# Kernel tuning notes

Hardware: AMD Instinct MI355X
Metric: run time of the kernel (lower is better)

The kernel has to match this reference:

```python
import jax, jax.numpy as jnp
import numpy as np

N, D = 8192, 1024


def setup_inputs() -> dict:
    key = jax.random.key(0)
    k1, k2, k3 = jax.random.split(key, 3)
    f_1 = jax.random.normal(k1, (N, D), dtype=jnp.float32)
    f_2 = jax.random.normal(k2, (N, D), dtype=jnp.float32)
    f_3 = jax.random.normal(k3, (N, D), dtype=jnp.float32)
    return {"f_1": f_1, "f_2": f_2, "f_3": f_3, "batch": 3}


def _svdvals(x):
    # torch.svd computes full U, S, V; only singular values are consumed.
    return jnp.linalg.svd(x, compute_uv=False)


def reference(f_1, f_2, f_3, batch):
    if batch == 2:
        s_1 = _svdvals(f_1)
        if f_2.shape[0] == 0:
            return s_1[0] ** 2
        s_2 = _svdvals(f_2)
        return s_1.mean() + s_2.mean()
    elif batch == 3:
        s_1 = _svdvals(f_1)
        s_2 = _svdvals(f_2)
        s_3 = _svdvals(f_3)
        return s_1[0] ** 2 + 0.5 * (s_2[0] ** 2 + s_3[0] ** 2)
```

## Files before the change

### kernel.cpp

```cpp
#include <hip/hip_runtime.h>


#define DIM 1024
#define NROW 8192
#define MSZ (DIM*DIM)
#define NS 5

typedef __attribute__((ext_vector_type(8))) short short8;
typedef __attribute__((ext_vector_type(4))) float f32x4;

__device__ inline float bf2f(unsigned short u) {
    union { unsigned i; float f; } x; x.i = ((unsigned)u) << 16; return x.f;
}
__device__ inline unsigned short f2bf(float f) {
    union { float f; unsigned i; } x; x.f = f;
    unsigned r = x.i + 0x7FFFu + ((x.i >> 16) & 1u);
    return (unsigned short)(r >> 16);
}
__device__ inline void gload16(const void* g, void* l) {
    __builtin_amdgcn_global_load_lds(
        (const __attribute__((address_space(1))) unsigned int*)g,
        (__attribute__((address_space(3))) unsigned int*)l, 16, 0, 0);
}

__global__ __launch_bounds__(256)
void tconv_k(const float* __restrict__ f0, const float* __restrict__ f1,
             const float* __restrict__ f2, unsigned short* __restrict__ ft) {
    const int m = blockIdx.z;
    const float* f = (m == 0) ? f0 : (m == 1 ? f1 : f2);
    unsigned short* o = ft + (size_t)m * DIM * NROW;
    __shared__ float T[64][68];
    const int c0 = blockIdx.x * 64, r0 = blockIdx.y * 64;
    const int tid = threadIdx.x;
    const int cx = (tid & 15) * 4, ry = tid >> 4;
#pragma unroll
    for (int i = 0; i < 4; ++i) {
        int r = ry + i * 16;
        float4 v = *(const float4*)&f[(size_t)(r0 + r) * DIM + c0 + cx];
        T[cx + 0][r] = v.x;
        T[cx + 1][r] = v.y;
        T[cx + 2][r] = v.z;
        T[cx + 3][r] = v.w;
    }
    __syncthreads();
#pragma unroll
    for (int i = 0; i < 4; ++i) {
        int c = ry + i * 16;
        float4 g = *(const float4*)&T[c][cx];
        ushort4 u;
        u.x = f2bf(g.x); u.y = f2bf(g.y); u.z = f2bf(g.z); u.w = f2bf(g.w);
        *(ushort4*)&o[(size_t)(c0 + c) * NROW + r0 + cx] = u;
    }
}

__global__ __launch_bounds__(256)
void syrk_sk(const unsigned short* __restrict__ src, float* __restrict__ Gp) {
    const int b = blockIdx.x;
    const int ky = b & 3;
    const int q = b >> 2;
    const int m = q / 36;
    const int tile = q - m * 36;
    int idx = tile, ti = 0;
    while (idx >= 8 - ti) { idx -= 8 - ti; ++ti; }
    const int tj = ti + idx;
    const int i0 = ti * 128, j0 = tj * 128;
    const unsigned short* S = src + (size_t)m * DIM * NROW;
    float* G = Gp + ((size_t)m * 36 + tile) * 16384;
    const int k0b = ky << 11;

    __shared__ unsigned short As[2 * 128 * 32];
    __shared__ unsigned short Bs[2 * 128 * 32];

    const int tid = threadIdx.x, w = tid >> 6, lane = tid & 63;
    const int wi = w >> 1, wj = w & 1;

    f32x4 acc[4][4];
#pragma unroll
    for (int a = 0; a < 4; ++a)
#pragma unroll
        for (int c = 0; c < 4; ++c) acc[a][c] = (f32x4){0.f, 0.f, 0.f, 0.f};

    const int lr = lane >> 2;
    const int ksw = (((lane & 3) ^ ((lane >> 4) & 3)) * 8);
    const int fr = lane & 15;
    const int slot = (((lane >> 4) ^ ((fr >> 2) & 3)) * 8);

    for (int k0 = k0b; k0 < k0b + 2048; k0 += 64) {
#pragma unroll
        for (int h = 0; h < 2; ++h)
#pragma unroll
            for (int p = 0; p < 2; ++p) {
                int rr = w * 32 + p * 16;
                gload16(S + (size_t)(i0 + rr + lr) * NROW + k0 + h * 32 + ksw,
                        &As[h * 4096 + rr * 32]);
                gload16(S + (size_t)(j0 + rr + lr) * NROW + k0 + h * 32 + ksw,
                        &Bs[h * 4096 + rr * 32]);
            }
        __syncthreads();
#pragma unroll
        for (int h = 0; h < 2; ++h) {
            short8 af[4], bfv[4];
#pragma unroll
            for (int a = 0; a < 4; ++a)
                af[a] = *(const short8*)&As[h * 4096 + (wi * 64 + a * 16 + fr) * 32 + slot];
#pragma unroll
            for (int c = 0; c < 4; ++c)
                bfv[c] = *(const short8*)&Bs[h * 4096 + (wj * 64 + c * 16 + fr) * 32 + slot];
#pragma unroll
            for (int a = 0; a < 4; ++a)
#pragma unroll
                for (int c = 0; c < 4; ++c)
                    acc[a][c] = __builtin_amdgcn_mfma_f32_16x16x32_bf16(
                        af[a], bfv[c], acc[a][c], 0, 0, 0);
        }
        __syncthreads();
    }

    const int qr = (lane >> 4) * 4, cn = lane & 15;
#pragma unroll
    for (int a = 0; a < 4; ++a)
#pragma unroll
        for (int c = 0; c < 4; ++c) {
            int cl = wj * 64 + c * 16 + cn;
#pragma unroll
            for (int reg = 0; reg < 4; ++reg) {
                int rl = wi * 64 + a * 16 + qr + reg;
                atomicAdd(&G[rl * 128 + cl], acc[a][c][reg]);
            }
        }
}

__global__ __launch_bounds__(256)
void convert_k(const float* __restrict__ Gp, float* __restrict__ trout,
               unsigned short* __restrict__ dst) {
    const int m = blockIdx.z;
    int idx = blockIdx.x, ti = 0;
    while (idx >= 8 - ti) { idx -= 8 - ti; ++ti; }
    const int tj = ti + idx;
    const int i0 = ti * 128, j0 = tj * 128;
    const float* G = Gp + ((size_t)m * 36 + blockIdx.x) * 16384;
    unsigned short* D = dst + (size_t)m * MSZ;
    __shared__ unsigned short T[128][136];
    const int tid = threadIdx.x;
    const int cx = (tid & 31) * 4, ry = tid >> 5;
    float dtr = 0.f;
#pragma unroll 4
    for (int t = 0; t < 16; ++t) {
        int r = ry + t * 8;
        float4 g = *(const float4*)&G[r * 128 + cx];
        ushort4 o;
        o.x = f2bf(g.x); o.y = f2bf(g.y); o.z = f2bf(g.z); o.w = f2bf(g.w);
        *(ushort4*)&D[(size_t)(i0 + r) * DIM + j0 + cx] = o;
        int rs = r ^ (cx & 124);
        T[cx + 0][rs] = o.x; T[cx + 1][rs] = o.y;
        T[cx + 2][rs] = o.z; T[cx + 3][rs] = o.w;
        if (ti == tj) {
            int d = r - cx;
            if (d >= 0 && d < 4)
                dtr += (d == 0 ? g.x : d == 1 ? g.y : d == 2 ? g.z : g.w);
        }
    }
    if (ti == tj) atomicAdd(&trout[m], dtr);
    if (ti != tj) {
        __syncthreads();
#pragma unroll 4
        for (int t = 0; t < 16; ++t) {
            int p = ry + t * 8;
            int qs = cx ^ (p & 124);
            ushort4 o = *(const ushort4*)&T[p][qs];
            *(ushort4*)&D[(size_t)(j0 + p) * DIM + i0 + cx] = o;
        }
    }
}

__global__ __launch_bounds__(256)
void sq_k(const unsigned short* __restrict__ src, const float* __restrict__ trin,
          float* __restrict__ trout, unsigned short* __restrict__ dst) {
    const int m = blockIdx.z;
    const unsigned short* S = src + (size_t)m * MSZ;
    unsigned short* D = dst + (size_t)m * MSZ;
    int idx = blockIdx.x, ti = 0;
    while (idx >= 16 - ti) { idx -= 16 - ti; ++ti; }
    const int tj = ti + idx;
    const int i0 = ti * 64, j0 = tj * 64;
    float tv = trin[m];
    const float sc = 1.f / (tv * tv);

    __shared__ unsigned short As[2 * 64 * 32];
    __shared__ unsigned short Bs[2 * 64 * 32];
    __shared__ unsigned short Ts[64][68];

    const int tid = threadIdx.x, w = tid >> 6, lane = tid & 63;
    const int wi = w >> 1, wj = w & 1;
    f32x4 acc[2][2];
#pragma unroll
    for (int a = 0; a < 2; ++a)
#pragma unroll
        for (int b = 0; b < 2; ++b) acc[a][b] = (f32x4){0.f, 0.f, 0.f, 0.f};

    const int lr = lane >> 2;
    const int ksw = (((lane & 3) ^ ((lane >> 4) & 3)) * 8);
    const int fr = lane & 15;
    const int slot = (((lane >> 4) ^ ((fr >> 2) & 3)) * 8);

    for (int k0 = 0; k0 < DIM; k0 += 64) {
#pragma unroll
        for (int h = 0; h < 2; ++h) {
            gload16(S + (size_t)(i0 + w * 16 + lr) * DIM + k0 + h * 32 + ksw,
                    &As[h * 2048 + w * 16 * 32]);
            gload16(S + (size_t)(j0 + w * 16 + lr) * DIM + k0 + h * 32 + ksw,
                    &Bs[h * 2048 + w * 16 * 32]);
        }
        __syncthreads();
#pragma unroll
        for (int h = 0; h < 2; ++h) {
            short8 af[2], bfv[2];
#pragma unroll
            for (int a = 0; a < 2; ++a)
                af[a] = *(const short8*)&As[h * 2048 + (wi * 32 + a * 16 + fr) * 32 + slot];
#pragma unroll
            for (int c = 0; c < 2; ++c)
                bfv[c] = *(const short8*)&Bs[h * 2048 + (wj * 32 + c * 16 + fr) * 32 + slot];
#pragma unroll
            for (int a = 0; a < 2; ++a)
#pragma unroll
                for (int c = 0; c < 2; ++c)
                    acc[a][c] = __builtin_amdgcn_mfma_f32_16x16x32_bf16(
                        af[a], bfv[c], acc[a][c], 0, 0, 0);
        }
        __syncthreads();
    }

    const int qr = (lane >> 4) * 4, cn = lane & 15;
#pragma unroll
    for (int a = 0; a < 2; ++a)
#pragma unroll
        for (int b = 0; b < 2; ++b) {
            int cl = wj * 32 + b * 16 + cn;
#pragma unroll
            for (int reg = 0; reg < 4; ++reg) {
                int rl = wi * 32 + a * 16 + qr + reg;
                unsigned short val = f2bf(acc[a][b][reg] * sc);
                D[(size_t)(i0 + rl) * DIM + j0 + cl] = val;
                Ts[cl][rl] = val;
            }
        }
    if (ti == tj && wi == wj) {
        int d = cn - qr;
        if (d >= 0 && d < 4)
            atomicAdd(&trout[m], (acc[0][0][d] + acc[1][1][d]) * sc);
    }
    if (ti != tj) {
        __syncthreads();
        const int cx = (tid & 15) * 4, ry = tid >> 4;
#pragma unroll
        for (int tq = 0; tq < 4; ++tq) {
            int p = ry + tq * 16;
            ushort4 o;
            o.x = Ts[p][cx + 0]; o.y = Ts[p][cx + 1];
            o.z = Ts[p][cx + 2]; o.w = Ts[p][cx + 3];
            *(ushort4*)&D[(size_t)(j0 + p) * DIM + i0 + cx] = o;
        }
    }
}

__global__ __launch_bounds__(256)
void mv_bf16(const unsigned short* __restrict__ M, const float* __restrict__ vin,
             float* __restrict__ vout) {
    int m = blockIdx.y;
    const unsigned short* A = M + (size_t)m * MSZ;
    int wv = threadIdx.x >> 6, lane = threadIdx.x & 63;
    int row = blockIdx.x * 4 + wv;
    const unsigned short* a = A + (size_t)row * DIM;
    float s = 0.f;
    if (vin) {
        const float* v = vin + m * DIM;
        for (int j = lane; j < DIM; j += 64) s += bf2f(a[j]) * v[j];
    } else {
        for (int j = lane; j < DIM; j += 64) s += bf2f(a[j]);
    }
    for (int off = 32; off; off >>= 1) s += __shfl_down(s, off);
    if (lane == 0) vout[m * DIM + row] = s;
}

__global__ __launch_bounds__(256)
void ray_k(const float* __restrict__ Gp, const float* __restrict__ wv,
           float* __restrict__ num) {
    const int m = blockIdx.y;
    int idx = blockIdx.x, ti = 0;
    while (idx >= 8 - ti) { idx -= 8 - ti; ++ti; }
    const int tj = ti + idx;
    const float* G = Gp + ((size_t)m * 36 + blockIdx.x) * 16384;
    const float* wi = wv + m * DIM + ti * 128;
    const float* wj = wv + m * DIM + tj * 128;
    const int tid = threadIdx.x;
    const int r = tid >> 1, c0 = (tid & 1) * 64;
    float inner = 0.f;
    const float4* g4 = (const float4*)&G[r * 128 + c0];
    const float4* w4 = (const float4*)&wj[c0];
#pragma unroll
    for (int t = 0; t < 16; ++t) {
        float4 g = g4[t], ww = w4[t];
        inner += g.x * ww.x + g.y * ww.y + g.z * ww.z + g.w * ww.w;
    }
    float s = wi[r] * inner;
    for (int off = 32; off; off >>= 1) s += __shfl_down(s, off);
    __shared__ float part[4];
    int lane = tid & 63, wx = tid >> 6;
    if (lane == 0) part[wx] = s;
    __syncthreads();
    if (tid == 0) {
        float tot = part[0] + part[1] + part[2] + part[3];
        if (ti != tj) tot *= 2.f;
        atomicAdd(&num[m], tot);
    }
}

__global__ __launch_bounds__(256)
void final_k(const float* __restrict__ num, const float* __restrict__ w,
             float* __restrict__ out) {
    __shared__ float red[256];
    int tid = threadIdx.x;
    float lam[3];
    for (int m = 0; m < 3; ++m) {
        float s = 0.f;
        for (int i = tid; i < DIM; i += 256) { float x = w[m * DIM + i]; s += x * x; }
        red[tid] = s; __syncthreads();
        for (int off = 128; off; off >>= 1) {
            if (tid < off) red[tid] += red[tid + off];
            __syncthreads();
        }
        lam[m] = num[m] / red[0]; __syncthreads();
    }
    if (tid == 0) out[0] = lam[0] + 0.5f * (lam[1] + lam[2]);
}

extern "C" void kernel_launch(void* const* d_in, const int* in_sizes, int n_in,
                              void* d_out, int out_size, void* d_ws, size_t ws_size,
                              hipStream_t stream) {
    const float* f0 = (const float*)d_in[0];
    const float* f1 = (const float*)d_in[1];
    const float* f2 = (const float*)d_in[2];

    char* base = (char*)d_ws;
    unsigned short* ft = (unsigned short*)base;
    unsigned short* Q  = (unsigned short*)base;
    unsigned short* P  = (unsigned short*)(base + 50331648);
    float* G32 = (float*)(base + 56623104);
    float* trbuf = (float*)(base + 63700992);
    float* num = trbuf + 40;
    float* v = (float*)(base + 63701248);
    float* w = v + 3 * DIM;

    hipMemsetAsync(G32, 0, 7078144, stream);

    dim3 gt(DIM / 64, NROW / 64, 3);
    tconv_k<<<gt, 256, 0, stream>>>(f0, f1, f2, ft);

    syrk_sk<<<432, 256, 0, stream>>>(ft, G32);
    convert_k<<<dim3(36, 1, 3), 256, 0, stream>>>(G32, trbuf, P);

    unsigned short* cur = P;
    unsigned short* nxt = Q;
    for (int s = 0; s < NS; ++s) {
        sq_k<<<dim3(136, 1, 3), 256, 0, stream>>>(cur, trbuf + s * 3,
                                                  trbuf + (s + 1) * 3, nxt);
        unsigned short* t2 = cur; cur = nxt; nxt = t2;
    }

    dim3 b(256, 1, 1);
    dim3 gm(DIM / 4, 3, 1);
    mv_bf16<<<gm, b, 0, stream>>>(cur, nullptr, v);
    mv_bf16<<<gm, b, 0, stream>>>(cur, v, w);

    ray_k<<<dim3(36, 3, 1), 256, 0, stream>>>(G32, w, num);
    final_k<<<1, 256, 0, stream>>>(num, w, (float*)d_out);
}
```

Before: 289.8 us.

## Fuse memset, first mat-vec, and final reduction into neighboring kernels

The workspace zeroing moves into the transpose kernel, so the separate memset launch goes away. The last squaring kernel now also computes row sums, which stand in for the first mat-vec against the all-ones vector. The second mat-vec accumulates the squared norm, and the Rayleigh kernel computes the final scalar with a last-block atomic counter, which removes the final kernel. This cuts three launches and one full matrix read, at the cost of extra shared-memory atomics in sq_k. Row sums are now taken from unrounded fp32 values instead of the bf16-rounded matrix.

Result: slower. 298.5 us (+3.0%).

```diff
diff --git a/kernel.cpp b/kernel.cpp
--- a/kernel.cpp
+++ b/kernel.cpp
@@ -5,6 +5,7 @@
 #define NROW 8192
 #define MSZ (DIM*DIM)
 #define NS 5
+#define NZ4 443148
 
 typedef __attribute__((ext_vector_type(8))) short short8;
 typedef __attribute__((ext_vector_type(4))) float f32x4;
@@ -25,13 +26,20 @@
 
 __global__ __launch_bounds__(256)
 void tconv_k(const float* __restrict__ f0, const float* __restrict__ f1,
-             const float* __restrict__ f2, unsigned short* __restrict__ ft) {
+             const float* __restrict__ f2, unsigned short* __restrict__ ft,
+             float* __restrict__ zbase) {
     const int m = blockIdx.z;
+    const int tid = threadIdx.x;
+    if (m == 0) {
+        int flat = blockIdx.x + 16 * blockIdx.y;
+        size_t i = (size_t)flat * 217 + tid;
+        if (tid < 217 && i < NZ4)
+            ((float4*)zbase)[i] = make_float4(0.f, 0.f, 0.f, 0.f);
+    }
     const float* f = (m == 0) ? f0 : (m == 1 ? f1 : f2);
     unsigned short* o = ft + (size_t)m * DIM * NROW;
     __shared__ float T[64][68];
     const int c0 = blockIdx.x * 64, r0 = blockIdx.y * 64;
-    const int tid = threadIdx.x;
     const int cx = (tid & 15) * 4, ry = tid >> 4;
 #pragma unroll
     for (int i = 0; i < 4; ++i) {
@@ -175,7 +183,8 @@
 
 __global__ __launch_bounds__(256)
 void sq_k(const unsigned short* __restrict__ src, const float* __restrict__ trin,
-          float* __restrict__ trout, unsigned short* __restrict__ dst) {
+          float* __restrict__ trout, unsigned short* __restrict__ dst,
+          float* __restrict__ vout) {
     const int m = blockIdx.z;
     const unsigned short* S = src + (size_t)m * MSZ;
     unsigned short* D = dst + (size_t)m * MSZ;
@@ -189,6 +198,7 @@
     __shared__ unsigned short As[2 * 64 * 32];
     __shared__ unsigned short Bs[2 * 64 * 32];
     __shared__ unsigned short Ts[64][68];
+    __shared__ float rs[64], cs[64];
 
     const int tid = threadIdx.x, w = tid >> 6, lane = tid & 63;
     const int wi = w >> 1, wj = w & 1;
@@ -231,7 +241,15 @@
         __syncthreads();
     }
 
+    if (vout) {
+        if (tid < 64) rs[tid] = 0.f;
+        else if (tid < 128) cs[tid - 64] = 0.f;
+        __syncthreads();
+    }
+
     const int qr = (lane >> 4) * 4, cn = lane & 15;
+    float rsum[2][4] = {{0.f, 0.f, 0.f, 0.f}, {0.f, 0.f, 0.f, 0.f}};
+    float csum[2] = {0.f, 0.f};
 #pragma unroll
     for (int a = 0; a < 2; ++a)
 #pragma unroll
@@ -240,11 +258,26 @@
 #pragma unroll
             for (int reg = 0; reg < 4; ++reg) {
                 int rl = wi * 32 + a * 16 + qr + reg;
-                unsigned short val = f2bf(acc[a][b][reg] * sc);
+                float vv = acc[a][b][reg] * sc;
+                unsigned short val = f2bf(vv);
                 D[(size_t)(i0 + rl) * DIM + j0 + cl] = val;
                 Ts[cl][rl] = val;
+                rsum[a][reg] += vv;
+                csum[b] += vv;
             }
         }
+    if (vout) {
+#pragma unroll
+        for (int a = 0; a < 2; ++a)
+#pragma unroll
+            for (int reg = 0; reg < 4; ++reg)
+                atomicAdd(&rs[wi * 32 + a * 16 + qr + reg], rsum[a][reg]);
+        if (ti != tj) {
+#pragma unroll
+            for (int b = 0; b < 2; ++b)
+                atomicAdd(&cs[wj * 32 + b * 16 + cn], csum[b]);
+        }
+    }
     if (ti == tj && wi == wj) {
         int d = cn - qr;
         if (d >= 0 && d < 4)
@@ -262,30 +295,37 @@
             *(ushort4*)&D[(size_t)(j0 + p) * DIM + i0 + cx] = o;
         }
     }
+    if (vout) {
+        __syncthreads();
+        if (tid < 64) atomicAdd(&vout[m * DIM + i0 + tid], rs[tid]);
+        else if (tid < 128 && ti != tj)
+            atomicAdd(&vout[m * DIM + j0 + tid - 64], cs[tid - 64]);
+    }
 }
 
 __global__ __launch_bounds__(256)
 void mv_bf16(const unsigned short* __restrict__ M, const float* __restrict__ vin,
-             float* __restrict__ vout) {
+             float* __restrict__ vout, float* __restrict__ den) {
     int m = blockIdx.y;
     const unsigned short* A = M + (size_t)m * MSZ;
     int wv = threadIdx.x >> 6, lane = threadIdx.x & 63;
     int row = blockIdx.x * 4 + wv;
     const unsigned short* a = A + (size_t)row * DIM;
+    const float* v = vin + m * DIM;
     float s = 0.f;
-    if (vin) {
-        const float* v = vin + m * DIM;
-        for (int j = lane; j < DIM; j += 64) s += bf2f(a[j]) * v[j];
-    } else {
-        for (int j = lane; j < DIM; j += 64) s += bf2f(a[j]);
-    }
+    for (int j = lane; j < DIM; j += 64) s += bf2f(a[j]) * v[j];
     for (int off = 32; off; off >>= 1) s += __shfl_down(s, off);
-    if (lane == 0) vout[m * DIM + row] = s;
-}
-
-__global__ __launch_bounds__(256)
-void ray_k(const float* __restrict__ Gp, const float* __restrict__ wv,
-           float* __restrict__ num) {
+    __shared__ float part[4];
+    if (lane == 0) { vout[m * DIM + row] = s; part[wv] = s * s; }
+    __syncthreads();
+    if (threadIdx.x == 0)
+        atomicAdd(&den[m], part[0] + part[1] + part[2] + part[3]);
+}
+
+__global__ __launch_bounds__(256)
+void rayfinal_k(const float* __restrict__ Gp, const float* __restrict__ wv,
+                float* __restrict__ num, float* __restrict__ den,
+                unsigned int* __restrict__ ctr, float* __restrict__ out) {
     const int m = blockIdx.y;
     int idx = blockIdx.x, ti = 0;
     while (idx >= 8 - ti) { idx -= 8 - ti; ++ti; }
@@ -313,26 +353,16 @@
         float tot = part[0] + part[1] + part[2] + part[3];
         if (ti != tj) tot *= 2.f;
         atomicAdd(&num[m], tot);
-    }
-}
-
-__global__ __launch_bounds__(256)
-void final_k(const float* __restrict__ num, const float* __restrict__ w,
-             float* __restrict__ out) {
-    __shared__ float red[256];
-    int tid = threadIdx.x;
-    float lam[3];
-    for (int m = 0; m < 3; ++m) {
-        float s = 0.f;
-        for (int i = tid; i < DIM; i += 256) { float x = w[m * DIM + i]; s += x * x; }
-        red[tid] = s; __syncthreads();
-        for (int off = 128; off; off >>= 1) {
-            if (tid < off) red[tid] += red[tid + off];
-            __syncthreads();
-        }
-        lam[m] = num[m] / red[0]; __syncthreads();
-    }
-    if (tid == 0) out[0] = lam[0] + 0.5f * (lam[1] + lam[2]);
+        __threadfence();
+        unsigned int old = atomicAdd(ctr, 1u);
+        if (old == 107u) {
+            float n0 = atomicAdd(&num[0], 0.f), n1 = atomicAdd(&num[1], 0.f);
+            float n2 = atomicAdd(&num[2], 0.f);
+            float d0 = atomicAdd(&den[0], 0.f), d1 = atomicAdd(&den[1], 0.f);
+            float d2 = atomicAdd(&den[2], 0.f);
+            out[0] = n0 / d0 + 0.5f * (n1 / d1 + n2 / d2);
+        }
+    }
 }
 
 extern "C" void kernel_launch(void* const* d_in, const int* in_sizes, int n_in,
@@ -347,15 +377,15 @@
     unsigned short* Q  = (unsigned short*)base;
     unsigned short* P  = (unsigned short*)(base + 50331648);
     float* G32 = (float*)(base + 56623104);
-    float* trbuf = (float*)(base + 63700992);
+    float* trbuf = G32 + 1769472;
     float* num = trbuf + 40;
-    float* v = (float*)(base + 63701248);
+    float* den = trbuf + 43;
+    unsigned int* ctr = (unsigned int*)(trbuf + 46);
+    float* v = trbuf + 48;
     float* w = v + 3 * DIM;
 
-    hipMemsetAsync(G32, 0, 7078144, stream);
-
     dim3 gt(DIM / 64, NROW / 64, 3);
-    tconv_k<<<gt, 256, 0, stream>>>(f0, f1, f2, ft);
+    tconv_k<<<gt, 256, 0, stream>>>(f0, f1, f2, ft, G32);
 
     syrk_sk<<<432, 256, 0, stream>>>(ft, G32);
     convert_k<<<dim3(36, 1, 3), 256, 0, stream>>>(G32, trbuf, P);
@@ -363,16 +393,15 @@
     unsigned short* cur = P;
     unsigned short* nxt = Q;
     for (int s = 0; s < NS; ++s) {
-        sq_k<<<dim3(136, 1, 3), 256, 0, stream>>>(cur, trbuf + s * 3,
-                                                  trbuf + (s + 1) * 3, nxt);
+        sq_k<<<dim3(136, 1, 3), 256, 0, stream>>>(
+            cur, trbuf + s * 3, trbuf + (s + 1) * 3, nxt,
+            (s == NS - 1) ? v : nullptr);
         unsigned short* t2 = cur; cur = nxt; nxt = t2;
     }
 
-    dim3 b(256, 1, 1);
     dim3 gm(DIM / 4, 3, 1);
-    mv_bf16<<<gm, b, 0, stream>>>(cur, nullptr, v);
-    mv_bf16<<<gm, b, 0, stream>>>(cur, v, w);
-
-    ray_k<<<dim3(36, 3, 1), 256, 0, stream>>>(G32, w, num);
-    final_k<<<1, 256, 0, stream>>>(num, w, (float*)d_out);
-}
+    mv_bf16<<<gm, 256, 0, stream>>>(cur, v, w, den);
+
+    rayfinal_k<<<dim3(36, 3, 1), 256, 0, stream>>>(G32, w, num, den, ctr,
+                                                   (float*)d_out);
+}
```
